# Kernel optimization log

Hardware: AMD Instinct MI355X
Metric: run time of the kernel (lower is better)

## Reference

```python
import jax, jax.numpy as jnp
import numpy as np

P = 16  # patch size
EPS = 1e-5  # LayerNorm eps (torch default)


def setup_inputs() -> dict:
    key = jax.random.key(0)
    ks = jax.random.split(key, 4)
    B, C, H, W = 64, 3, 384, 384
    ps, hid = C * P * P, 2 * C * P * P  # 768, 1536
    x = jax.random.normal(ks[0], (B, C, H, W), dtype=jnp.float32)
    ln_w = jnp.ones((ps,), jnp.float32)
    ln_b = jnp.zeros((ps,), jnp.float32)
    w1 = jax.random.normal(ks[1], (ps, hid), jnp.float32) * (1.0 / np.sqrt(ps))
    b1 = jnp.zeros((hid,), jnp.float32)
    w2 = jax.random.normal(ks[2], (hid, ps), jnp.float32) * (1.0 / np.sqrt(hid))
    b2 = jnp.zeros((ps,), jnp.float32)
    return {"x": x, "ln_w": ln_w, "ln_b": ln_b, "w1": w1, "b1": b1, "w2": w2, "b2": b2}


def reference(x, ln_w, ln_b, w1, b1, w2, b2):
    B, C, H, W = x.shape
    Hp, Wp = H // P, W // P
    ps = C * P * P
    # unfold with kernel=stride=P (non-overlapping): [B, L, C*P*P]
    # torch unfold channel ordering is (C, kh, kw) per patch, patches row-major.
    y = x.reshape(B, C, Hp, P, Wp, P).transpose(0, 2, 4, 1, 3, 5).reshape(B, Hp * Wp, ps)
    # LayerNorm over last dim
    mu = y.mean(-1, keepdims=True)
    var = ((y - mu) ** 2).mean(-1, keepdims=True)
    y = (y - mu) * jax.lax.rsqrt(var + EPS) * ln_w + ln_b
    # 2-layer MLP with exact GELU
    h = jax.nn.gelu(jnp.einsum('blp,ph->blh', y, w1) + b1, approximate=False)
    y = jnp.einsum('blh,hp->blp', h, w2) + b2
    # fold back (inverse of unfold for non-overlapping patches)
    y = y.reshape(B, Hp, Wp, C, P, P).transpose(0, 3, 1, 4, 2, 5).reshape(B, C, H, W)
    return x + y
```

## Files before the change

kernel.cpp:

```cpp
#include <hip/hip_runtime.h>
#include <hip/hip_bf16.h>
#include <stdint.h>


#define TOK   36864
#define PS    768
#define HID   1536
#define NPB   576
#define WPDIM 24

typedef __attribute__((ext_vector_type(8)))  short bf16x8_t;
typedef __attribute__((ext_vector_type(16))) float floatx16_t;

__device__ __forceinline__ ushort f2bf(float f) {
    union { __hip_bfloat16 h; ushort u; } cv;
    cv.h = __float2bfloat16(f);
    return cv.u;
}
__device__ __forceinline__ float bf2f(ushort u) {
    union { ushort u; __hip_bfloat16 h; } cv;
    cv.u = u;
    return __bfloat162float(cv.h);
}

__device__ __forceinline__ void gload16(const ushort* g, ushort* l) {
    __builtin_amdgcn_global_load_lds((__attribute__((address_space(1))) const void*)g,
                                     (__attribute__((address_space(3))) void*)l, 16, 0, 0);
}

__global__ __launch_bounds__(256)
void wsplit_transpose(const float* __restrict__ in, int K, int N,
                      ushort* __restrict__ outHi, ushort* __restrict__ outLo)
{
    __shared__ float tile[32][33];
    const int n0 = blockIdx.x * 32, k0 = blockIdx.y * 32;
    const int tx = threadIdx.x & 31, ty = threadIdx.x >> 5;
#pragma unroll
    for (int i = 0; i < 4; ++i) {
        const int kl = ty + i * 8;
        tile[kl][tx] = in[(size_t)(k0 + kl) * N + n0 + tx];
    }
    __syncthreads();
#pragma unroll
    for (int i = 0; i < 4; ++i) {
        const int nl = ty + i * 8;
        const float v = tile[tx][nl];
        const ushort hi = f2bf(v);
        const ushort lo = f2bf(v - bf2f(hi));
        const size_t o = (size_t)(n0 + nl) * K + k0 + tx;
        outHi[o] = hi;
        outLo[o] = lo;
    }
}

__global__ __launch_bounds__(256)
void patch_ln_kernel(const float* __restrict__ x, const float* __restrict__ lnw,
                     const float* __restrict__ lnb,
                     ushort* __restrict__ Yhi, ushort* __restrict__ Ylo)
{
    const int wave = threadIdx.x >> 6, lane = threadIdx.x & 63;
    const int t = blockIdx.x * 4 + wave;
    const int b  = t / NPB;
    const int l  = t - b * NPB;
    const int hp = l / WPDIM;
    const int wp = l - hp * WPDIM;
    const float* xb = x + (size_t)b * 3 * 384 * 384;

    float v[12];
    float s = 0.f, ss = 0.f;
#pragma unroll
    for (int w = 0; w < 3; ++w) {
        const int p  = w * 256 + lane * 4;
        const int c  = p >> 8, ph = (p >> 4) & 15, pw = p & 15;
        const float4 f = *(const float4*)(xb + (size_t)(c * 384 + hp * 16 + ph) * 384 + wp * 16 + pw);
        v[w*4+0] = f.x; v[w*4+1] = f.y; v[w*4+2] = f.z; v[w*4+3] = f.w;
        s  += f.x + f.y + f.z + f.w;
        ss += f.x*f.x + f.y*f.y + f.z*f.z + f.w*f.w;
    }
#pragma unroll
    for (int off = 32; off > 0; off >>= 1) {
        s  += __shfl_xor(s,  off);
        ss += __shfl_xor(ss, off);
    }
    const float mu = s * (1.f / 768.f);
    const float rs = rsqrtf(fmaxf(ss * (1.f / 768.f) - mu * mu, 0.f) + 1e-5f);

#pragma unroll
    for (int w = 0; w < 3; ++w) {
        const int p = w * 256 + lane * 4;
        const float4 gw = *(const float4*)(lnw + p);
        const float4 gb = *(const float4*)(lnb + p);
        union { ushort u[4]; uint2 q; } hi, lo;
        float yv;
        yv = (v[w*4+0] - mu) * rs * gw.x + gb.x; hi.u[0] = f2bf(yv); lo.u[0] = f2bf(yv - bf2f(hi.u[0]));
        yv = (v[w*4+1] - mu) * rs * gw.y + gb.y; hi.u[1] = f2bf(yv); lo.u[1] = f2bf(yv - bf2f(hi.u[1]));
        yv = (v[w*4+2] - mu) * rs * gw.z + gb.z; hi.u[2] = f2bf(yv); lo.u[2] = f2bf(yv - bf2f(hi.u[2]));
        yv = (v[w*4+3] - mu) * rs * gw.w + gb.w; hi.u[3] = f2bf(yv); lo.u[3] = f2bf(yv - bf2f(hi.u[3]));
        *(uint2*)(Yhi + (size_t)t * PS + p) = hi.q;
        *(uint2*)(Ylo + (size_t)t * PS + p) = lo.q;
    }
}

__device__ __forceinline__ void stage_ktile(
    const ushort* __restrict__ Ahi, const ushort* __restrict__ Alo,
    const ushort* __restrict__ Bhi, const ushort* __restrict__ Blo,
    ushort* lA_hi, ushort* lA_lo, ushort* lB_hi, ushort* lB_lo,
    int brow, int bcol, int K, int k0, int wave, int lane)
{
    const int r = lane >> 2;
    const int chunk = ((lane & 3) ^ ((lane >> 3) & 3)) * 8;
#pragma unroll
    for (int j = 0; j < 2; ++j) {
        const int row = j * 64 + wave * 16 + r;
        const size_t ga = (size_t)(brow + row) * K + k0 + chunk;
        const size_t gb = (size_t)(bcol + row) * K + k0 + chunk;
        const int lofs = (j * 64 + wave * 16) * 32;
        gload16(Ahi + ga, lA_hi + lofs);
        gload16(Alo + ga, lA_lo + lofs);
        gload16(Bhi + gb, lB_hi + lofs);
        gload16(Blo + gb, lB_lo + lofs);
    }
}

template<int DO_GELU>
__global__ __launch_bounds__(256, 2)
void gemm_bf16x3(const ushort* __restrict__ Ahi, const ushort* __restrict__ Alo,
                 const ushort* __restrict__ Bhi, const ushort* __restrict__ Blo,
                 const float* __restrict__ bias,
                 int M, int N, int K,
                 ushort* __restrict__ OutHi, ushort* __restrict__ OutLo,
                 const float* __restrict__ xres, float* __restrict__ out)
{
    __shared__ __align__(16) ushort lds[2][4][128 * 32];
    const int tid  = threadIdx.x;
    const int wave = tid >> 6, lane = tid & 63;
    const int brow = blockIdx.y * 128, bcol = blockIdx.x * 128;
    const int wr = (wave >> 1) * 64, wc = (wave & 1) * 64;

    floatx16_t acc[2][2];
#pragma unroll
    for (int i = 0; i < 2; ++i)
#pragma unroll
        for (int j = 0; j < 2; ++j)
#pragma unroll
            for (int e = 0; e < 16; ++e) acc[i][j][e] = 0.f;

    stage_ktile(Ahi, Alo, Bhi, Blo, lds[0][0], lds[0][1], lds[0][2], lds[0][3],
                brow, bcol, K, 0, wave, lane);
    __syncthreads();

    const int fr = lane & 31;
    const int kh = lane >> 5;
    const int sw = (fr >> 1) & 3;

    const int KT = K >> 5;
    int buf = 0;
    for (int kt = 0; kt < KT; ++kt) {
        if (kt + 1 < KT)
            stage_ktile(Ahi, Alo, Bhi, Blo,
                        lds[buf ^ 1][0], lds[buf ^ 1][1], lds[buf ^ 1][2], lds[buf ^ 1][3],
                        brow, bcol, K, (kt + 1) * 32, wave, lane);

        bf16x8_t ah[2][2], al[2][2], bh[2][2], bl[2][2];
#pragma unroll
        for (int mi = 0; mi < 2; ++mi)
#pragma unroll
            for (int s = 0; s < 2; ++s) {
                const int c = (s * 2 + kh) ^ sw;
                const int off = (wr + mi * 32 + fr) * 32 + c * 8;
                ah[mi][s] = *(const bf16x8_t*)&lds[buf][0][off];
                al[mi][s] = *(const bf16x8_t*)&lds[buf][1][off];
            }
#pragma unroll
        for (int ni = 0; ni < 2; ++ni)
#pragma unroll
            for (int s = 0; s < 2; ++s) {
                const int c = (s * 2 + kh) ^ sw;
                const int off = (wc + ni * 32 + fr) * 32 + c * 8;
                bh[ni][s] = *(const bf16x8_t*)&lds[buf][2][off];
                bl[ni][s] = *(const bf16x8_t*)&lds[buf][3][off];
            }
#pragma unroll
        for (int mi = 0; mi < 2; ++mi)
#pragma unroll
            for (int ni = 0; ni < 2; ++ni)
#pragma unroll
                for (int s = 0; s < 2; ++s) {
                    acc[mi][ni] = __builtin_amdgcn_mfma_f32_32x32x16_bf16(ah[mi][s], bh[ni][s], acc[mi][ni], 0, 0, 0);
                    acc[mi][ni] = __builtin_amdgcn_mfma_f32_32x32x16_bf16(ah[mi][s], bl[ni][s], acc[mi][ni], 0, 0, 0);
                    acc[mi][ni] = __builtin_amdgcn_mfma_f32_32x32x16_bf16(al[mi][s], bh[ni][s], acc[mi][ni], 0, 0, 0);
                }
        __syncthreads();
        buf ^= 1;
    }

    const int ocol  = lane & 31;
    const int orow4 = (lane >> 5) * 4;
#pragma unroll
    for (int mi = 0; mi < 2; ++mi) {
#pragma unroll
        for (int ni = 0; ni < 2; ++ni) {
            const int col = bcol + wc + ni * 32 + ocol;
            const float bv = bias[col];
#pragma unroll
            for (int reg = 0; reg < 16; ++reg) {
                const int row = brow + wr + mi * 32 + orow4 + (reg & 3) + 8 * (reg >> 2);
                float v = acc[mi][ni][reg] + bv;
                if (DO_GELU) {
                    v = 0.5f * v * (1.0f + erff(v * 0.70710678118654752f));
                    const ushort hi = f2bf(v);
                    const ushort lo = f2bf(v - bf2f(hi));
                    const size_t o = (size_t)row * N + col;
                    OutHi[o] = hi;
                    OutLo[o] = lo;
                } else {
                    const int t  = row;
                    const int b  = t / NPB;
                    const int l  = t - b * NPB;
                    const int hp = l / WPDIM;
                    const int wp = l - hp * WPDIM;
                    const int c  = col >> 8, ph = (col >> 4) & 15, pw = col & 15;
                    const size_t idx = ((size_t)(b * 3 + c) * 384 + hp * 16 + ph) * 384 + wp * 16 + pw;
                    out[idx] = xres[idx] + v;
                }
            }
        }
    }
}

extern "C" void kernel_launch(void* const* d_in, const int* in_sizes, int n_in,
                              void* d_out, int out_size, void* d_ws, size_t ws_size,
                              hipStream_t stream)
{
    const float* x   = (const float*)d_in[0];
    const float* lnw = (const float*)d_in[1];
    const float* lnb = (const float*)d_in[2];
    const float* w1  = (const float*)d_in[3];
    const float* b1  = (const float*)d_in[4];
    const float* w2  = (const float*)d_in[5];
    const float* b2  = (const float*)d_in[6];
    float* out = (float*)d_out;

    char* ws = (char*)d_ws;
    size_t o = 0;
    ushort* Yhi  = (ushort*)(ws + o); o += (size_t)TOK * PS * 2;
    ushort* Ylo  = (ushort*)(ws + o); o += (size_t)TOK * PS * 2;
    ushort* W1h  = (ushort*)(ws + o); o += (size_t)PS * HID * 2;
    ushort* W1l  = (ushort*)(ws + o); o += (size_t)PS * HID * 2;
    ushort* W2h  = (ushort*)(ws + o); o += (size_t)HID * PS * 2;
    ushort* W2l  = (ushort*)(ws + o); o += (size_t)HID * PS * 2;
    ushort* Hh   = (ushort*)(ws + o); o += (size_t)TOK * HID * 2;
    ushort* Hl   = (ushort*)(ws + o); o += (size_t)TOK * HID * 2;

    wsplit_transpose<<<dim3(HID / 32, PS / 32), 256, 0, stream>>>(w1, PS, HID, W1h, W1l);
    wsplit_transpose<<<dim3(PS / 32, HID / 32), 256, 0, stream>>>(w2, HID, PS, W2h, W2l);

    patch_ln_kernel<<<TOK / 4, 256, 0, stream>>>(x, lnw, lnb, Yhi, Ylo);

    gemm_bf16x3<1><<<dim3(HID / 128, TOK / 128), 256, 0, stream>>>(
        Yhi, Ylo, W1h, W1l, b1, TOK, HID, PS, Hh, Hl, nullptr, nullptr);

    gemm_bf16x3<0><<<dim3(PS / 128, TOK / 128), 256, 0, stream>>>(
        Hh, Hl, W2h, W2l, b2, TOK, PS, HID, nullptr, nullptr, x, out);
}
```

Baseline: 920.4 us.

## Rework bf16x3 GEMMs to 256x256 tiles with 8 waves and XCD-aware block mapping

Replaces the 128x128, 4-wave GEMM with a 256x256-tile, 8-wave (512-thread) kernel. Hi and lo halves are staged into one interleaved 64-wide LDS row with an XOR swizzle. Block IDs are remapped so that consecutive tiles group per XCD for better L2 reuse. The K loop uses explicit vmcnt waits, raw s_barrier, sched_barriers and setprio around the MFMA bursts, which overlaps global-to-LDS loads with compute and raises arithmetic intensity per LDS byte. The risks are that occupancy drops to one block per CU with a large register accumulator set, and that the hand-coded waitcnt/barrier ordering is fragile.

```diff
diff --git a/kernel.cpp b/kernel.cpp
--- a/kernel.cpp
+++ b/kernel.cpp
@@ -27,6 +27,8 @@
     __builtin_amdgcn_global_load_lds((__attribute__((address_space(1))) const void*)g,
                                      (__attribute__((address_space(3))) void*)l, 16, 0, 0);
 }
+
+#define SCB() __builtin_amdgcn_sched_barrier(0)
 
 __global__ __launch_bounds__(256)
 void wsplit_transpose(const float* __restrict__ in, int K, int N,
@@ -101,110 +103,121 @@
     }
 }
 
-__device__ __forceinline__ void stage_ktile(
-    const ushort* __restrict__ Ahi, const ushort* __restrict__ Alo,
-    const ushort* __restrict__ Bhi, const ushort* __restrict__ Blo,
-    ushort* lA_hi, ushort* lA_lo, ushort* lB_hi, ushort* lB_lo,
-    int brow, int bcol, int K, int k0, int wave, int lane)
-{
-    const int r = lane >> 2;
-    const int chunk = ((lane & 3) ^ ((lane >> 3) & 3)) * 8;
-#pragma unroll
-    for (int j = 0; j < 2; ++j) {
-        const int row = j * 64 + wave * 16 + r;
-        const size_t ga = (size_t)(brow + row) * K + k0 + chunk;
-        const size_t gb = (size_t)(bcol + row) * K + k0 + chunk;
-        const int lofs = (j * 64 + wave * 16) * 32;
-        gload16(Ahi + ga, lA_hi + lofs);
-        gload16(Alo + ga, lA_lo + lofs);
-        gload16(Bhi + gb, lB_hi + lofs);
-        gload16(Blo + gb, lB_lo + lofs);
-    }
-}
-
 template<int DO_GELU>
-__global__ __launch_bounds__(256, 2)
-void gemm_bf16x3(const ushort* __restrict__ Ahi, const ushort* __restrict__ Alo,
-                 const ushort* __restrict__ Bhi, const ushort* __restrict__ Blo,
-                 const float* __restrict__ bias,
-                 int M, int N, int K,
-                 ushort* __restrict__ OutHi, ushort* __restrict__ OutLo,
-                 const float* __restrict__ xres, float* __restrict__ out)
-{
-    __shared__ __align__(16) ushort lds[2][4][128 * 32];
+__global__ __launch_bounds__(512, 1)
+void gemm_bf16x3_8p(const ushort* __restrict__ Ahi, const ushort* __restrict__ Alo,
+                    const ushort* __restrict__ Bhi, const ushort* __restrict__ Blo,
+                    const float* __restrict__ bias,
+                    int M, int N, int K, int nbx,
+                    ushort* __restrict__ OutHi, ushort* __restrict__ OutLo,
+                    const float* __restrict__ xres, float* __restrict__ out)
+{
+    __shared__ __align__(16) ushort lds[2][2][256 * 64];
     const int tid  = threadIdx.x;
     const int wave = tid >> 6, lane = tid & 63;
-    const int brow = blockIdx.y * 128, bcol = blockIdx.x * 128;
-    const int wr = (wave >> 1) * 64, wc = (wave & 1) * 64;
-
-    floatx16_t acc[2][2];
-#pragma unroll
-    for (int i = 0; i < 2; ++i)
-#pragma unroll
-        for (int j = 0; j < 2; ++j)
-#pragma unroll
-            for (int e = 0; e < 16; ++e) acc[i][j][e] = 0.f;
-
-    stage_ktile(Ahi, Alo, Bhi, Blo, lds[0][0], lds[0][1], lds[0][2], lds[0][3],
-                brow, bcol, K, 0, wave, lane);
-    __syncthreads();
+
+    const int nwg = gridDim.x;
+    const int wg  = (blockIdx.x & 7) * (nwg >> 3) + (blockIdx.x >> 3);
+    const int bx  = wg % nbx, by = wg / nbx;
+    const int brow = by * 256, bcol = bx * 256;
+
+    const int wrm = wave >> 2;
+    const int wrn = wave & 3;
+
+    const int rb = wave * 32;
+    const int lr = lane >> 3, sl = lane & 7;
+    const int g  = sl ^ lr;
+    const int go = (g & 3) * 8;
+    const ushort* PA = (g < 4) ? Ahi : Alo;
+    const ushort* PB = (g < 4) ? Bhi : Blo;
+
+    floatx16_t acc[4][2];
+#pragma unroll
+    for (int mi = 0; mi < 4; ++mi)
+#pragma unroll
+        for (int ni = 0; ni < 2; ++ni)
+#pragma unroll
+            for (int e = 0; e < 16; ++e) acc[mi][ni][e] = 0.f;
+
+    const int KT = K >> 5;
+
+#pragma unroll
+    for (int i = 0; i < 4; ++i) {
+        const int r = rb + i * 8 + lr;
+        gload16(PA + (size_t)(brow + r) * K + go, (ushort*)&lds[0][0][(rb + i * 8) * 64]);
+        gload16(PB + (size_t)(bcol + r) * K + go, (ushort*)&lds[0][1][(rb + i * 8) * 64]);
+    }
+    SCB();
 
     const int fr = lane & 31;
     const int kh = lane >> 5;
-    const int sw = (fr >> 1) & 3;
-
-    const int KT = K >> 5;
-    int buf = 0;
-    for (int kt = 0; kt < KT; ++kt) {
-        if (kt + 1 < KT)
-            stage_ktile(Ahi, Alo, Bhi, Blo,
-                        lds[buf ^ 1][0], lds[buf ^ 1][1], lds[buf ^ 1][2], lds[buf ^ 1][3],
-                        brow, bcol, K, (kt + 1) * 32, wave, lane);
-
-        bf16x8_t ah[2][2], al[2][2], bh[2][2], bl[2][2];
-#pragma unroll
-        for (int mi = 0; mi < 2; ++mi)
-#pragma unroll
-            for (int s = 0; s < 2; ++s) {
-                const int c = (s * 2 + kh) ^ sw;
-                const int off = (wr + mi * 32 + fr) * 32 + c * 8;
-                ah[mi][s] = *(const bf16x8_t*)&lds[buf][0][off];
-                al[mi][s] = *(const bf16x8_t*)&lds[buf][1][off];
-            }
-#pragma unroll
-        for (int ni = 0; ni < 2; ++ni)
-#pragma unroll
-            for (int s = 0; s < 2; ++s) {
-                const int c = (s * 2 + kh) ^ sw;
-                const int off = (wc + ni * 32 + fr) * 32 + c * 8;
-                bh[ni][s] = *(const bf16x8_t*)&lds[buf][2][off];
-                bl[ni][s] = *(const bf16x8_t*)&lds[buf][3][off];
-            }
-#pragma unroll
-        for (int mi = 0; mi < 2; ++mi)
-#pragma unroll
-            for (int ni = 0; ni < 2; ++ni)
-#pragma unroll
-                for (int s = 0; s < 2; ++s) {
-                    acc[mi][ni] = __builtin_amdgcn_mfma_f32_32x32x16_bf16(ah[mi][s], bh[ni][s], acc[mi][ni], 0, 0, 0);
-                    acc[mi][ni] = __builtin_amdgcn_mfma_f32_32x32x16_bf16(ah[mi][s], bl[ni][s], acc[mi][ni], 0, 0, 0);
-                    acc[mi][ni] = __builtin_amdgcn_mfma_f32_32x32x16_bf16(al[mi][s], bh[ni][s], acc[mi][ni], 0, 0, 0);
+    const int sx = fr & 7;
+
+    for (int t = 0; t < KT; ++t) {
+        const int cur = t & 1;
+        if (t + 1 < KT) {
+            const int k0 = (t + 1) * 32;
+#pragma unroll
+            for (int i = 0; i < 4; ++i) {
+                const int r = rb + i * 8 + lr;
+                gload16(PA + (size_t)(brow + r) * K + k0 + go, (ushort*)&lds[cur ^ 1][0][(rb + i * 8) * 64]);
+                gload16(PB + (size_t)(bcol + r) * K + k0 + go, (ushort*)&lds[cur ^ 1][1][(rb + i * 8) * 64]);
+            }
+            SCB();
+            asm volatile("s_waitcnt vmcnt(8)" ::: "memory");
+        } else {
+            SCB();
+            asm volatile("s_waitcnt vmcnt(0)" ::: "memory");
+        }
+        SCB();
+        __builtin_amdgcn_s_barrier();
+        SCB();
+
+#pragma unroll
+        for (int s = 0; s < 2; ++s) {
+            bf16x8_t ah[4], al[4], bh[2], bl[2];
+            const int sh  = (s * 2 + kh) ^ sx;
+            const int slo = (4 + s * 2 + kh) ^ sx;
+#pragma unroll
+            for (int mi = 0; mi < 4; ++mi) {
+                const int R = wrm * 128 + mi * 32 + fr;
+                ah[mi] = *(const bf16x8_t*)&lds[cur][0][R * 64 + sh * 8];
+                al[mi] = *(const bf16x8_t*)&lds[cur][0][R * 64 + slo * 8];
+            }
+#pragma unroll
+            for (int ni = 0; ni < 2; ++ni) {
+                const int R = wrn * 64 + ni * 32 + fr;
+                bh[ni] = *(const bf16x8_t*)&lds[cur][1][R * 64 + sh * 8];
+                bl[ni] = *(const bf16x8_t*)&lds[cur][1][R * 64 + slo * 8];
+            }
+            __builtin_amdgcn_s_setprio(1);
+#pragma unroll
+            for (int mi = 0; mi < 4; ++mi)
+#pragma unroll
+                for (int ni = 0; ni < 2; ++ni) {
+                    acc[mi][ni] = __builtin_amdgcn_mfma_f32_32x32x16_bf16(ah[mi], bh[ni], acc[mi][ni], 0, 0, 0);
+                    acc[mi][ni] = __builtin_amdgcn_mfma_f32_32x32x16_bf16(ah[mi], bl[ni], acc[mi][ni], 0, 0, 0);
+                    acc[mi][ni] = __builtin_amdgcn_mfma_f32_32x32x16_bf16(al[mi], bh[ni], acc[mi][ni], 0, 0, 0);
                 }
-        __syncthreads();
-        buf ^= 1;
-    }
-
-    const int ocol  = lane & 31;
-    const int orow4 = (lane >> 5) * 4;
-#pragma unroll
-    for (int mi = 0; mi < 2; ++mi) {
+            __builtin_amdgcn_s_setprio(0);
+        }
+        asm volatile("s_waitcnt lgkmcnt(0)" ::: "memory");
+        SCB();
+        __builtin_amdgcn_s_barrier();
+        SCB();
+    }
+
+    const int ocol = lane & 31;
+    const int or4  = kh * 4;
+#pragma unroll
+    for (int mi = 0; mi < 4; ++mi) {
 #pragma unroll
         for (int ni = 0; ni < 2; ++ni) {
-            const int col = bcol + wc + ni * 32 + ocol;
+            const int col = bcol + wrn * 64 + ni * 32 + ocol;
             const float bv = bias[col];
 #pragma unroll
             for (int reg = 0; reg < 16; ++reg) {
-                const int row = brow + wr + mi * 32 + orow4 + (reg & 3) + 8 * (reg >> 2);
+                const int row = brow + wrm * 128 + mi * 32 + or4 + (reg & 3) + 8 * (reg >> 2);
                 float v = acc[mi][ni][reg] + bv;
                 if (DO_GELU) {
                     v = 0.5f * v * (1.0f + erff(v * 0.70710678118654752f));
@@ -214,9 +227,9 @@
                     OutHi[o] = hi;
                     OutLo[o] = lo;
                 } else {
-                    const int t  = row;
-                    const int b  = t / NPB;
-                    const int l  = t - b * NPB;
+                    const int tk = row;
+                    const int b  = tk / NPB;
+                    const int l  = tk - b * NPB;
                     const int hp = l / WPDIM;
                     const int wp = l - hp * WPDIM;
                     const int c  = col >> 8, ph = (col >> 4) & 15, pw = col & 15;
@@ -257,9 +270,9 @@
 
     patch_ln_kernel<<<TOK / 4, 256, 0, stream>>>(x, lnw, lnb, Yhi, Ylo);
 
-    gemm_bf16x3<1><<<dim3(HID / 128, TOK / 128), 256, 0, stream>>>(
-        Yhi, Ylo, W1h, W1l, b1, TOK, HID, PS, Hh, Hl, nullptr, nullptr);
-
-    gemm_bf16x3<0><<<dim3(PS / 128, TOK / 128), 256, 0, stream>>>(
-        Hh, Hl, W2h, W2l, b2, TOK, PS, HID, nullptr, nullptr, x, out);
-}
+    gemm_bf16x3_8p<1><<<(HID / 256) * (TOK / 256), 512, 0, stream>>>(
+        Yhi, Ylo, W1h, W1l, b1, TOK, HID, PS, HID / 256, Hh, Hl, nullptr, nullptr);
+
+    gemm_bf16x3_8p<0><<<(PS / 256) * (TOK / 256), 512, 0, stream>>>(
+        Hh, Hl, W2h, W2l, b2, TOK, PS, HID, PS / 256, nullptr, nullptr, x, out);
+}
```

Result: faster. 888.7 us (-3.4%).
